# Kernel optimization log

Hardware: AMD Instinct MI355X
Metric: run time of the kernel (lower is better)

## Reference

```python
import jax, jax.numpy as jnp
import numpy as np

TABLE_SIZE = 256
N_EMBD = 768
B, T = 2, 1024
VOCAB = TABLE_SIZE * TABLE_SIZE


def setup_inputs() -> dict:
    key = jax.random.key(0)
    k1, k2, k3, k4 = jax.random.split(key, 4)
    hidden_states = jax.random.normal(k1, (B, T, N_EMBD), dtype=jnp.float32)
    target_ids = jax.random.randint(k2, (B, T), 0, VOCAB, dtype=jnp.int32).astype(jnp.int64)
    W_row = jax.random.normal(k3, (TABLE_SIZE, N_EMBD), dtype=jnp.float32) * 0.02
    b_row = jnp.zeros((TABLE_SIZE,), dtype=jnp.float32)
    col_weight = jax.random.normal(k4, (TABLE_SIZE, N_EMBD, TABLE_SIZE), dtype=jnp.float32) * 0.02
    col_bias = jnp.zeros((TABLE_SIZE, TABLE_SIZE), dtype=jnp.float32)
    return {
        "hidden_states": hidden_states,
        "target_ids": target_ids,
        "W_row": W_row,
        "b_row": b_row,
        "col_weight": col_weight,
        "col_bias": col_bias,
    }


def reference(hidden_states, target_ids, W_row, b_row, col_weight, col_bias):
    table_size = col_weight.shape[0]
    # row head: (B,T,R)
    row_logits = jnp.einsum("btd,rd->btr", hidden_states, W_row) + b_row
    # codebook.lookup: factor token id over table_size x table_size grid
    row_ids = (target_ids // table_size).reshape(-1)  # (N,)
    col_ids = (target_ids % table_size).reshape(-1)   # (N,)
    hs_flat = hidden_states.reshape(-1, hidden_states.shape[-1])  # (N,d)
    # per-token hard-routed column projection (the gather + baddbmm)
    W_tok = col_weight[row_ids]                       # (N,d,C)
    col_logits = jnp.einsum("nd,ndc->nc", hs_flat, W_tok) + col_bias[row_ids]
    # cross-entropy losses (mean over tokens)
    lp_row = jax.nn.log_softmax(row_logits.reshape(-1, table_size), axis=-1)
    loss_row = -jnp.take_along_axis(lp_row, row_ids[:, None], axis=1).mean()
    lp_col = jax.nn.log_softmax(col_logits, axis=-1)
    loss_col = -jnp.take_along_axis(lp_col, col_ids[:, None], axis=1).mean()
    return loss_row + loss_col
```

## Files before the change

kernel.cpp:

```cpp
#include <hip/hip_runtime.h>
#include <math.h>

#define TABLE 256
#define DIM   768
#define NCH   6
#define DCH   128
#define KTOK  12
#define CAP   64

__device__ __forceinline__ float2 f2zero() { return make_float2(0.f, 0.f); }

__global__ __launch_bounds__(256) void k_ztrans(
    const float* __restrict__ Wrow,
    float* __restrict__ WrowT,
    int* __restrict__ counts)
{
    const int d = blockIdx.x;
    const int c = threadIdx.x;
    if (d == 0) counts[c] = 0;
    WrowT[(size_t)d * TABLE + c] = Wrow[(size_t)c * DIM + d];
}

__global__ __launch_bounds__(256) void k_bucket(
    const int* __restrict__ tgt, int ntok,
    int* __restrict__ counts, int* __restrict__ bucket)
{
    const int n = blockIdx.x * 256 + threadIdx.x;
    if (n >= ntok) return;
    const int r = tgt[n] >> 8;
    const int pos = atomicAdd(&counts[r], 1);
    if (pos < CAP) bucket[r * CAP + pos] = n;
}

__device__ __forceinline__ void stream_pass(
    const float* __restrict__ slab,
    const float* __restrict__ hs,
    const int* tk,
    int nvalid,
    int dbase,
    int cbase,
    float* __restrict__ outp,
    int lane)
{
    int off[KTOK];
    #pragma unroll
    for (int j = 0; j < KTOK; ++j) off[j] = tk[j] * DIM + dbase;

    float2 acc[KTOK];
    #pragma unroll
    for (int j = 0; j < KTOK; ++j) acc[j] = f2zero();

    const float* sl = slab + cbase + 2 * lane;

    #pragma unroll 2
    for (int dq = 0; dq < DCH / 4; ++dq) {
        float4 hv[KTOK];
        #pragma unroll
        for (int j = 0; j < KTOK; ++j)
            hv[j] = reinterpret_cast<const float4*>(hs + off[j])[dq];
        #pragma unroll
        for (int dd = 0; dd < 4; ++dd) {
            const float2 wv = *reinterpret_cast<const float2*>(
                sl + (size_t)(dq * 4 + dd) * TABLE);
            #pragma unroll
            for (int j = 0; j < KTOK; ++j) {
                const float h = (dd == 0) ? hv[j].x : (dd == 1) ? hv[j].y
                              : (dd == 2) ? hv[j].z : hv[j].w;
                acc[j].x = fmaf(h, wv.x, acc[j].x);
                acc[j].y = fmaf(h, wv.y, acc[j].y);
            }
        }
    }

    #pragma unroll
    for (int j = 0; j < KTOK; ++j)
        if (j < nvalid)
            *reinterpret_cast<float2*>(outp + (size_t)tk[j] * TABLE + cbase + 2 * lane)
                = acc[j];
}

__global__ __launch_bounds__(64) void k_stream(
    const float* __restrict__ hs,
    const float* __restrict__ WrowT,
    const float* __restrict__ CW,
    const int* __restrict__ counts,
    const int* __restrict__ bucket,
    float* __restrict__ row_part,
    float* __restrict__ col_part,
    int ntok)
{
    const int bid  = blockIdx.x;
    const int lane = threadIdx.x;
    const int ncol = 256 * NCH * 2;
    int tk[KTOK];

    if (bid < ncol) {
        const int r     = bid & 255;
        const int rest  = bid >> 8;
        const int chunk = rest >> 1;
        const int cbase = (rest & 1) * 128;
        const int cnt = min(counts[r], CAP);
        if (cnt == 0) return;
        const float* slab = CW + (size_t)r * DIM * TABLE + (size_t)chunk * DCH * TABLE;
        float* outp = col_part + (size_t)chunk * ntok * TABLE;
        for (int base = 0; base < cnt; base += KTOK) {
            #pragma unroll
            for (int j = 0; j < KTOK; ++j) {
                const int idx = (base + j < cnt) ? (base + j) : base;
                tk[j] = __builtin_amdgcn_readfirstlane(bucket[r * CAP + idx]);
            }
            stream_pass(slab, hs, tk, min(KTOK, cnt - base),
                        chunk * DCH, cbase, outp, lane);
        }
    } else {
        const int b      = bid - ncol;
        const int ntiles = (ntok + KTOK - 1) / KTOK;
        const int tile   = b % ntiles;
        const int rest   = b / ntiles;
        const int chunk  = rest >> 1;
        const int cbase  = (rest & 1) * 128;
        const int cnt    = min(KTOK, ntok - tile * KTOK);
        #pragma unroll
        for (int j = 0; j < KTOK; ++j) {
            const int idx = (j < cnt) ? j : 0;
            tk[j] = tile * KTOK + idx;
        }
        const float* slab = WrowT + (size_t)chunk * DCH * TABLE;
        float* outp = row_part + (size_t)chunk * ntok * TABLE;
        stream_pass(slab, hs, tk, cnt, chunk * DCH, cbase, outp, lane);
    }
}

__device__ __forceinline__ float wave_nll(float4 v, int target, int lane) {
    float m = fmaxf(fmaxf(v.x, v.y), fmaxf(v.z, v.w));
    #pragma unroll
    for (int off = 32; off > 0; off >>= 1) m = fmaxf(m, __shfl_xor(m, off));
    float e = expf(v.x - m) + expf(v.y - m) + expf(v.z - m) + expf(v.w - m);
    float lt = 0.f;
    if (lane == (target >> 2)) {
        const int j = target & 3;
        lt = (j == 0) ? v.x : (j == 1) ? v.y : (j == 2) ? v.z : v.w;
    }
    #pragma unroll
    for (int off = 32; off > 0; off >>= 1) {
        e  += __shfl_xor(e, off);
        lt += __shfl_xor(lt, off);
    }
    return m + logf(e) - lt;
}

__global__ __launch_bounds__(256) void k_nll2(
    const float* __restrict__ row_part,
    const float* __restrict__ col_part,
    const float* __restrict__ brow,
    const float* __restrict__ cbias,
    const int* __restrict__ tgt, int ntok,
    float* __restrict__ per_tok)
{
    const int n = blockIdx.x * 4 + (threadIdx.x >> 6);
    if (n >= ntok) return;
    const int lane = threadIdx.x & 63;
    const int t = tgt[n];
    const int r = t >> 8;

    float4 rl = reinterpret_cast<const float4*>(brow)[lane];
    float4 cl = reinterpret_cast<const float4*>(cbias + (size_t)r * TABLE)[lane];
    #pragma unroll
    for (int ch = 0; ch < NCH; ++ch) {
        const float4 a = reinterpret_cast<const float4*>(
            row_part + ((size_t)ch * ntok + n) * TABLE)[lane];
        const float4 b = reinterpret_cast<const float4*>(
            col_part + ((size_t)ch * ntok + n) * TABLE)[lane];
        rl.x += a.x; rl.y += a.y; rl.z += a.z; rl.w += a.w;
        cl.x += b.x; cl.y += b.y; cl.z += b.z; cl.w += b.w;
    }
    const float lr = wave_nll(rl, r, lane);
    const float lc = wave_nll(cl, t & 255, lane);
    if (lane == 0) per_tok[n] = lr + lc;
}

__global__ __launch_bounds__(256) void k_reduce(
    const float* __restrict__ per_tok, int ntok, float* __restrict__ out)
{
    __shared__ float red[256];
    const int c = threadIdx.x;
    float s = 0.f;
    for (int i = c; i < ntok; i += 256) s += per_tok[i];
    red[c] = s;
    __syncthreads();
    #pragma unroll
    for (int k = 128; k > 0; k >>= 1) {
        if (c < k) red[c] += red[c + k];
        __syncthreads();
    }
    if (c == 0) out[0] = red[0] / (float)ntok;
}

extern "C" void kernel_launch(void* const* d_in, const int* in_sizes, int n_in,
                              void* d_out, int out_size, void* d_ws, size_t ws_size,
                              hipStream_t stream) {
    const float* hs    = (const float*)d_in[0];
    const int*   tgt   = (const int*)d_in[1];
    const float* Wrow  = (const float*)d_in[2];
    const float* brow  = (const float*)d_in[3];
    const float* CW    = (const float*)d_in[4];
    const float* cbias = (const float*)d_in[5];
    float* out = (float*)d_out;

    const int ntok = in_sizes[1];

    char* ws = (char*)d_ws;
    int*   counts   = (int*)(ws);
    int*   bucket   = (int*)(ws + 1024);
    float* WrowT    = (float*)(ws + 1024 + 256 * CAP * 4);
    char*  p0       = (char*)WrowT + (size_t)DIM * TABLE * 4;
    float* row_part = (float*)p0;
    float* col_part = row_part + (size_t)NCH * ntok * TABLE;
    float* per_tok  = col_part + (size_t)NCH * ntok * TABLE;

    const int ntiles = (ntok + KTOK - 1) / KTOK;
    const int nblk   = 256 * NCH * 2 + ntiles * NCH * 2;

    k_ztrans <<<DIM, 256, 0, stream>>>(Wrow, WrowT, counts);
    k_bucket <<<(ntok + 255) / 256, 256, 0, stream>>>(tgt, ntok, counts, bucket);
    k_stream <<<nblk, 64, 0, stream>>>(hs, WrowT, CW, counts, bucket,
                                       row_part, col_part, ntok);
    k_nll2   <<<(ntok + 3) / 4, 256, 0, stream>>>(row_part, col_part, brow, cbias,
                                                  tgt, ntok, per_tok);
    k_reduce <<<1, 256, 0, stream>>>(per_tok, ntok, out);
}
```

Measured before the change: 76.27 us.

## Pack four waves per block and compute row logits over full dim

The streaming kernel now runs four independent wave-tasks per 256-thread block instead of one 64-thread block per task. The row-head tasks no longer split the hidden dimension into six chunks with partial sums. Each wave computes the full 768-length dot product and writes final row logits, so the NLL kernel reads one row buffer instead of summing six partials. This cuts row partial-buffer traffic and launch granularity, but leaves fewer, longer row tasks that may load-balance worse against the column tasks.

```diff
diff --git a/kernel.cpp b/kernel.cpp
--- a/kernel.cpp
+++ b/kernel.cpp
@@ -32,6 +32,7 @@
     if (pos < CAP) bucket[r * CAP + pos] = n;
 }
 
+template<int NDQ>
 __device__ __forceinline__ void stream_pass(
     const float* __restrict__ slab,
     const float* __restrict__ hs,
@@ -53,7 +54,7 @@
     const float* sl = slab + cbase + 2 * lane;
 
     #pragma unroll 2
-    for (int dq = 0; dq < DCH / 4; ++dq) {
+    for (int dq = 0; dq < NDQ; ++dq) {
         float4 hv[KTOK];
         #pragma unroll
         for (int j = 0; j < KTOK; ++j)
@@ -79,24 +80,25 @@
                 = acc[j];
 }
 
-__global__ __launch_bounds__(64) void k_stream(
+__global__ __launch_bounds__(256) void k_stream(
     const float* __restrict__ hs,
     const float* __restrict__ WrowT,
     const float* __restrict__ CW,
     const int* __restrict__ counts,
     const int* __restrict__ bucket,
-    float* __restrict__ row_part,
+    float* __restrict__ row_logits,
     float* __restrict__ col_part,
     int ntok)
 {
-    const int bid  = blockIdx.x;
-    const int lane = threadIdx.x;
+    const int gw   = blockIdx.x * 4 + (threadIdx.x >> 6);
+    const int lane = threadIdx.x & 63;
     const int ncol = 256 * NCH * 2;
+    const int ntiles = (ntok + KTOK - 1) / KTOK;
     int tk[KTOK];
 
-    if (bid < ncol) {
-        const int r     = bid & 255;
-        const int rest  = bid >> 8;
+    if (gw < ncol) {
+        const int r     = gw & 255;
+        const int rest  = gw >> 8;
         const int chunk = rest >> 1;
         const int cbase = (rest & 1) * 128;
         const int cnt = min(counts[r], CAP);
@@ -109,25 +111,20 @@
                 const int idx = (base + j < cnt) ? (base + j) : base;
                 tk[j] = __builtin_amdgcn_readfirstlane(bucket[r * CAP + idx]);
             }
-            stream_pass(slab, hs, tk, min(KTOK, cnt - base),
-                        chunk * DCH, cbase, outp, lane);
+            stream_pass<DCH / 4>(slab, hs, tk, min(KTOK, cnt - base),
+                                 chunk * DCH, cbase, outp, lane);
         }
-    } else {
-        const int b      = bid - ncol;
-        const int ntiles = (ntok + KTOK - 1) / KTOK;
-        const int tile   = b % ntiles;
-        const int rest   = b / ntiles;
-        const int chunk  = rest >> 1;
-        const int cbase  = (rest & 1) * 128;
-        const int cnt    = min(KTOK, ntok - tile * KTOK);
+    } else if (gw < ncol + 2 * ntiles) {
+        const int t     = gw - ncol;
+        const int tile  = t >> 1;
+        const int cbase = (t & 1) * 128;
+        const int cnt   = min(KTOK, ntok - tile * KTOK);
         #pragma unroll
         for (int j = 0; j < KTOK; ++j) {
             const int idx = (j < cnt) ? j : 0;
             tk[j] = tile * KTOK + idx;
         }
-        const float* slab = WrowT + (size_t)chunk * DCH * TABLE;
-        float* outp = row_part + (size_t)chunk * ntok * TABLE;
-        stream_pass(slab, hs, tk, cnt, chunk * DCH, cbase, outp, lane);
+        stream_pass<DIM / 4>(WrowT, hs, tk, cnt, 0, cbase, row_logits, lane);
     }
 }
 
@@ -150,7 +147,7 @@
 }
 
 __global__ __launch_bounds__(256) void k_nll2(
-    const float* __restrict__ row_part,
+    const float* __restrict__ row_logits,
     const float* __restrict__ col_part,
     const float* __restrict__ brow,
     const float* __restrict__ cbias,
@@ -164,14 +161,16 @@
     const int r = t >> 8;
 
     float4 rl = reinterpret_cast<const float4*>(brow)[lane];
+    {
+        const float4 a = reinterpret_cast<const float4*>(
+            row_logits + (size_t)n * TABLE)[lane];
+        rl.x += a.x; rl.y += a.y; rl.z += a.z; rl.w += a.w;
+    }
     float4 cl = reinterpret_cast<const float4*>(cbias + (size_t)r * TABLE)[lane];
     #pragma unroll
     for (int ch = 0; ch < NCH; ++ch) {
-        const float4 a = reinterpret_cast<const float4*>(
-            row_part + ((size_t)ch * ntok + n) * TABLE)[lane];
         const float4 b = reinterpret_cast<const float4*>(
             col_part + ((size_t)ch * ntok + n) * TABLE)[lane];
-        rl.x += a.x; rl.y += a.y; rl.z += a.z; rl.w += a.w;
         cl.x += b.x; cl.y += b.y; cl.z += b.z; cl.w += b.w;
     }
     const float lr = wave_nll(rl, r, lane);
@@ -210,22 +209,23 @@
     const int ntok = in_sizes[1];
 
     char* ws = (char*)d_ws;
-    int*   counts   = (int*)(ws);
-    int*   bucket   = (int*)(ws + 1024);
-    float* WrowT    = (float*)(ws + 1024 + 256 * CAP * 4);
-    char*  p0       = (char*)WrowT + (size_t)DIM * TABLE * 4;
-    float* row_part = (float*)p0;
-    float* col_part = row_part + (size_t)NCH * ntok * TABLE;
-    float* per_tok  = col_part + (size_t)NCH * ntok * TABLE;
+    int*   counts     = (int*)(ws);
+    int*   bucket     = (int*)(ws + 1024);
+    float* WrowT      = (float*)(ws + 1024 + 256 * CAP * 4);
+    char*  p0         = (char*)WrowT + (size_t)DIM * TABLE * 4;
+    float* row_logits = (float*)p0;
+    float* col_part   = row_logits + (size_t)ntok * TABLE;
+    float* per_tok    = col_part + (size_t)NCH * ntok * TABLE;
 
     const int ntiles = (ntok + KTOK - 1) / KTOK;
-    const int nblk   = 256 * NCH * 2 + ntiles * NCH * 2;
+    const int nwaves = 256 * NCH * 2 + 2 * ntiles;
+    const int nblk   = (nwaves + 3) / 4;
 
     k_ztrans <<<DIM, 256, 0, stream>>>(Wrow, WrowT, counts);
     k_bucket <<<(ntok + 255) / 256, 256, 0, stream>>>(tgt, ntok, counts, bucket);
-    k_stream <<<nblk, 64, 0, stream>>>(hs, WrowT, CW, counts, bucket,
-                                       row_part, col_part, ntok);
-    k_nll2   <<<(ntok + 3) / 4, 256, 0, stream>>>(row_part, col_part, brow, cbias,
+    k_stream <<<nblk, 256, 0, stream>>>(hs, WrowT, CW, counts, bucket,
+                                        row_logits, col_part, ntok);
+    k_nll2   <<<(ntok + 3) / 4, 256, 0, stream>>>(row_logits, col_part, brow, cbias,
                                                   tgt, ntok, per_tok);
     k_reduce <<<1, 256, 0, stream>>>(per_tok, ntok, out);
 }
```

Result: slower. 265.8 us (+248.5%).

## Split column chunks finer and stage token hidden states in LDS

Applied to the files above, without the earlier changes.

Halves the d-chunk size for the column-weight streaming blocks (12 chunks of 64 instead of 6 of 128), doubling the number of column blocks so more of the GPU streams col_weight in parallel. Each pass now cooperatively loads the token hidden-state slices into LDS first and then reads them as broadcasts, instead of every lane issuing redundant uniform global loads. The cost is more partial-sum traffic: the column partial buffer doubles and the NLL kernel has to sum 12 column partials. Barriers are also added around each LDS staging step.

```diff
diff --git a/kernel.cpp b/kernel.cpp
--- a/kernel.cpp
+++ b/kernel.cpp
@@ -3,8 +3,10 @@
 
 #define TABLE 256
 #define DIM   768
-#define NCH   6
-#define DCH   128
+#define NCH_C 12
+#define NCH_R 6
+#define DCH_C 64
+#define DCH_R 128
 #define KTOK  12
 #define CAP   64
 
@@ -32,6 +34,7 @@
     if (pos < CAP) bucket[r * CAP + pos] = n;
 }
 
+template<int DCHT>
 __device__ __forceinline__ void stream_pass(
     const float* __restrict__ slab,
     const float* __restrict__ hs,
@@ -39,12 +42,23 @@
     int nvalid,
     int dbase,
     int cbase,
+    float* hs_lds,
     float* __restrict__ outp,
     int lane)
 {
-    int off[KTOK];
-    #pragma unroll
-    for (int j = 0; j < KTOK; ++j) off[j] = tk[j] * DIM + dbase;
+    constexpr int QPT = DCHT / 4;
+    constexpr int TPI = 64 / QPT;
+    const int sub = lane / QPT;
+    const int q   = lane % QPT;
+    __syncthreads();
+    #pragma unroll
+    for (int i = 0; i < KTOK / TPI; ++i) {
+        const int j = i * TPI + sub;
+        const float4 v = *reinterpret_cast<const float4*>(
+            hs + (size_t)tk[j] * DIM + dbase + 4 * q);
+        *reinterpret_cast<float4*>(hs_lds + j * DCHT + 4 * q) = v;
+    }
+    __syncthreads();
 
     float2 acc[KTOK];
     #pragma unroll
@@ -53,11 +67,11 @@
     const float* sl = slab + cbase + 2 * lane;
 
     #pragma unroll 2
-    for (int dq = 0; dq < DCH / 4; ++dq) {
+    for (int dq = 0; dq < DCHT / 4; ++dq) {
         float4 hv[KTOK];
         #pragma unroll
         for (int j = 0; j < KTOK; ++j)
-            hv[j] = reinterpret_cast<const float4*>(hs + off[j])[dq];
+            hv[j] = *reinterpret_cast<const float4*>(hs_lds + j * DCHT + 4 * dq);
         #pragma unroll
         for (int dd = 0; dd < 4; ++dd) {
             const float2 wv = *reinterpret_cast<const float2*>(
@@ -89,9 +103,11 @@
     float* __restrict__ col_part,
     int ntok)
 {
+    __shared__ float hs_lds[KTOK * DCH_R];
+
     const int bid  = blockIdx.x;
     const int lane = threadIdx.x;
-    const int ncol = 256 * NCH * 2;
+    const int ncol = 256 * NCH_C * 2;
     int tk[KTOK];
 
     if (bid < ncol) {
@@ -101,7 +117,7 @@
         const int cbase = (rest & 1) * 128;
         const int cnt = min(counts[r], CAP);
         if (cnt == 0) return;
-        const float* slab = CW + (size_t)r * DIM * TABLE + (size_t)chunk * DCH * TABLE;
+        const float* slab = CW + (size_t)r * DIM * TABLE + (size_t)chunk * DCH_C * TABLE;
         float* outp = col_part + (size_t)chunk * ntok * TABLE;
         for (int base = 0; base < cnt; base += KTOK) {
             #pragma unroll
@@ -109,12 +125,13 @@
                 const int idx = (base + j < cnt) ? (base + j) : base;
                 tk[j] = __builtin_amdgcn_readfirstlane(bucket[r * CAP + idx]);
             }
-            stream_pass(slab, hs, tk, min(KTOK, cnt - base),
-                        chunk * DCH, cbase, outp, lane);
+            stream_pass<DCH_C>(slab, hs, tk, min(KTOK, cnt - base),
+                               chunk * DCH_C, cbase, hs_lds, outp, lane);
         }
     } else {
         const int b      = bid - ncol;
         const int ntiles = (ntok + KTOK - 1) / KTOK;
+        if (b >= ntiles * NCH_R * 2) return;
         const int tile   = b % ntiles;
         const int rest   = b / ntiles;
         const int chunk  = rest >> 1;
@@ -125,9 +142,9 @@
             const int idx = (j < cnt) ? j : 0;
             tk[j] = tile * KTOK + idx;
         }
-        const float* slab = WrowT + (size_t)chunk * DCH * TABLE;
+        const float* slab = WrowT + (size_t)chunk * DCH_R * TABLE;
         float* outp = row_part + (size_t)chunk * ntok * TABLE;
-        stream_pass(slab, hs, tk, cnt, chunk * DCH, cbase, outp, lane);
+        stream_pass<DCH_R>(slab, hs, tk, cnt, chunk * DCH_R, cbase, hs_lds, outp, lane);
     }
 }
 
@@ -166,12 +183,15 @@
     float4 rl = reinterpret_cast<const float4*>(brow)[lane];
     float4 cl = reinterpret_cast<const float4*>(cbias + (size_t)r * TABLE)[lane];
     #pragma unroll
-    for (int ch = 0; ch < NCH; ++ch) {
+    for (int ch = 0; ch < NCH_R; ++ch) {
         const float4 a = reinterpret_cast<const float4*>(
             row_part + ((size_t)ch * ntok + n) * TABLE)[lane];
+        rl.x += a.x; rl.y += a.y; rl.z += a.z; rl.w += a.w;
+    }
+    #pragma unroll
+    for (int ch = 0; ch < NCH_C; ++ch) {
         const float4 b = reinterpret_cast<const float4*>(
             col_part + ((size_t)ch * ntok + n) * TABLE)[lane];
-        rl.x += a.x; rl.y += a.y; rl.z += a.z; rl.w += a.w;
         cl.x += b.x; cl.y += b.y; cl.z += b.z; cl.w += b.w;
     }
     const float lr = wave_nll(rl, r, lane);
@@ -215,11 +235,11 @@
     float* WrowT    = (float*)(ws + 1024 + 256 * CAP * 4);
     char*  p0       = (char*)WrowT + (size_t)DIM * TABLE * 4;
     float* row_part = (float*)p0;
-    float* col_part = row_part + (size_t)NCH * ntok * TABLE;
-    float* per_tok  = col_part + (size_t)NCH * ntok * TABLE;
+    float* col_part = row_part + (size_t)NCH_R * ntok * TABLE;
+    float* per_tok  = col_part + (size_t)NCH_C * ntok * TABLE;
 
     const int ntiles = (ntok + KTOK - 1) / KTOK;
-    const int nblk   = 256 * NCH * 2 + ntiles * NCH * 2;
+    const int nblk   = 256 * NCH_C * 2 + ntiles * NCH_R * 2;
 
     k_ztrans <<<DIM, 256, 0, stream>>>(Wrow, WrowT, counts);
     k_bucket <<<(ntok + 255) / 256, 256, 0, stream>>>(tgt, ntok, counts, bucket);
```

Measured after the change: 76.35 us. Within noise of the previous version (+0.1%).

## Merge column-half blocks into 128-thread blocks sharing hidden states via LDS

Applied to the files above, without the earlier changes.

Each stream block now has two waves that cover both 128-column halves, so the launch has half as many blocks. Per pass, the 12 tokens' hidden-state chunks are loaded once cooperatively into shared memory and read from there, instead of each wave loading them separately from global memory. This removes the duplicated hidden-state loads at the cost of two __syncthreads per pass and somewhat lower block-level parallelism.

```diff
diff --git a/kernel.cpp b/kernel.cpp
--- a/kernel.cpp
+++ b/kernel.cpp
@@ -38,13 +38,23 @@
     const int* tk,
     int nvalid,
     int dbase,
-    int cbase,
+    float* hs_lds,
     float* __restrict__ outp,
-    int lane)
-{
-    int off[KTOK];
-    #pragma unroll
-    for (int j = 0; j < KTOK; ++j) off[j] = tk[j] * DIM + dbase;
+    int tid)
+{
+    const int lane  = tid & 63;
+    const int cbase = (tid >> 6) * 128;
+
+    __syncthreads();
+    #pragma unroll
+    for (int i = 0; i < KTOK / 4; ++i) {
+        const int j = i * 4 + (tid >> 5);
+        const int q = tid & 31;
+        const float4 v = *reinterpret_cast<const float4*>(
+            hs + (size_t)tk[j] * DIM + dbase + 4 * q);
+        *reinterpret_cast<float4*>(hs_lds + j * DCH + 4 * q) = v;
+    }
+    __syncthreads();
 
     float2 acc[KTOK];
     #pragma unroll
@@ -57,7 +67,7 @@
         float4 hv[KTOK];
         #pragma unroll
         for (int j = 0; j < KTOK; ++j)
-            hv[j] = reinterpret_cast<const float4*>(hs + off[j])[dq];
+            hv[j] = *reinterpret_cast<const float4*>(hs_lds + j * DCH + 4 * dq);
         #pragma unroll
         for (int dd = 0; dd < 4; ++dd) {
             const float2 wv = *reinterpret_cast<const float2*>(
@@ -79,7 +89,7 @@
                 = acc[j];
 }
 
-__global__ __launch_bounds__(64) void k_stream(
+__global__ __launch_bounds__(128) void k_stream(
     const float* __restrict__ hs,
     const float* __restrict__ WrowT,
     const float* __restrict__ CW,
@@ -89,16 +99,16 @@
     float* __restrict__ col_part,
     int ntok)
 {
-    const int bid  = blockIdx.x;
-    const int lane = threadIdx.x;
-    const int ncol = 256 * NCH * 2;
+    __shared__ float hs_lds[KTOK * DCH];
+
+    const int bid = blockIdx.x;
+    const int tid = threadIdx.x;
+    const int ncol = 256 * NCH;
     int tk[KTOK];
 
     if (bid < ncol) {
         const int r     = bid & 255;
-        const int rest  = bid >> 8;
-        const int chunk = rest >> 1;
-        const int cbase = (rest & 1) * 128;
+        const int chunk = bid >> 8;
         const int cnt = min(counts[r], CAP);
         if (cnt == 0) return;
         const float* slab = CW + (size_t)r * DIM * TABLE + (size_t)chunk * DCH * TABLE;
@@ -110,15 +120,14 @@
                 tk[j] = __builtin_amdgcn_readfirstlane(bucket[r * CAP + idx]);
             }
             stream_pass(slab, hs, tk, min(KTOK, cnt - base),
-                        chunk * DCH, cbase, outp, lane);
+                        chunk * DCH, hs_lds, outp, tid);
         }
     } else {
         const int b      = bid - ncol;
         const int ntiles = (ntok + KTOK - 1) / KTOK;
+        if (b >= ntiles * NCH) return;
         const int tile   = b % ntiles;
-        const int rest   = b / ntiles;
-        const int chunk  = rest >> 1;
-        const int cbase  = (rest & 1) * 128;
+        const int chunk  = b / ntiles;
         const int cnt    = min(KTOK, ntok - tile * KTOK);
         #pragma unroll
         for (int j = 0; j < KTOK; ++j) {
@@ -127,7 +136,7 @@
         }
         const float* slab = WrowT + (size_t)chunk * DCH * TABLE;
         float* outp = row_part + (size_t)chunk * ntok * TABLE;
-        stream_pass(slab, hs, tk, cnt, chunk * DCH, cbase, outp, lane);
+        stream_pass(slab, hs, tk, cnt, chunk * DCH, hs_lds, outp, tid);
     }
 }
 
@@ -219,12 +228,12 @@
     float* per_tok  = col_part + (size_t)NCH * ntok * TABLE;
 
     const int ntiles = (ntok + KTOK - 1) / KTOK;
-    const int nblk   = 256 * NCH * 2 + ntiles * NCH * 2;
+    const int nblk   = 256 * NCH + ntiles * NCH;
 
     k_ztrans <<<DIM, 256, 0, stream>>>(Wrow, WrowT, counts);
     k_bucket <<<(ntok + 255) / 256, 256, 0, stream>>>(tgt, ntok, counts, bucket);
-    k_stream <<<nblk, 64, 0, stream>>>(hs, WrowT, CW, counts, bucket,
-                                       row_part, col_part, ntok);
+    k_stream <<<nblk, 128, 0, stream>>>(hs, WrowT, CW, counts, bucket,
+                                        row_part, col_part, ntok);
     k_nll2   <<<(ntok + 3) / 4, 256, 0, stream>>>(row_part, col_part, brow, cbias,
                                                   tgt, ntok, per_tok);
     k_reduce <<<1, 256, 0, stream>>>(per_tok, ntok, out);
```

Measured after the change: 72.63 us. 4.8% less time.
